# Performance work log

Measured on AMD Instinct MI355X. Metric: run time of the kernel, lower is better.

The kernel has to match this reference:

```python
import jax, jax.numpy as jnp
import numpy as np

B, R, D, H = 8192, 6, 1024, 256
TEMP = 0.5
SINKHORN_ITERS = 5


def rmsnorm(x, g, eps=1e-6):
    return x * jax.lax.rsqrt(jnp.mean(x * x, axis=-1, keepdims=True) + eps) * g


def setup_inputs() -> dict:
    key = jax.random.key(0)
    ks = jax.random.split(key, 24)
    def p(k, shape, fan):
        return jax.random.normal(k, shape, jnp.float32) / np.float32(np.sqrt(fan))
    return {
        'source_roles': jax.random.normal(ks[0], (B, R, D), jnp.float32),
        'target_roles': jax.random.normal(ks[1], (B, R, D), jnp.float32),
        # role_encoder: Linear(D,H) -> RMSNorm(H) -> SwiGLU(H, 2H) -> Linear(H,H)
        'W1': p(ks[2], (H, D), D), 'b1': jnp.zeros((H,), jnp.float32),
        'g1': jnp.ones((H,), jnp.float32),
        'Wa': p(ks[3], (2 * H, H), H),  # SwiGLU gate proj
        'Wb': p(ks[4], (2 * H, H), H),  # SwiGLU value proj
        'Wc': p(ks[5], (H, 2 * H), 2 * H),  # SwiGLU down proj
        'W2': p(ks[6], (H, H), H), 'b2': jnp.zeros((H,), jnp.float32),
        # map_score: Bilinear(H, H, 1)
        'Wbil': p(ks[7], (H, H), H), 'bbil': jnp.zeros((1,), jnp.float32),
        # answer_proj: Linear(2H,2H) -> GELU -> Linear(2H,D) -> RMSNorm(D)
        'Wa1': p(ks[8], (2 * H, 2 * H), 2 * H), 'ba1': jnp.zeros((2 * H,), jnp.float32),
        'Wa2': p(ks[9], (D, 2 * H), 2 * H), 'ba2': jnp.zeros((D,), jnp.float32),
        'g2': jnp.ones((D,), jnp.float32),
        # confidence_head: Linear(1,1) -> Sigmoid (input is a scalar statistic per batch)
        'Wc1': p(ks[10], (1, 1), 1), 'bc1': jnp.zeros((1,), jnp.float32),
    }


def reference(source_roles, target_roles, W1, b1, g1, Wa, Wb, Wc, W2, b2,
              Wbil, bbil, Wa1, ba1, Wa2, ba2, g2, Wc1, bc1):
    def role_encoder(x):  # [B,R,D] -> [B,R,H]
        x = x @ W1.T + b1
        x = rmsnorm(x, g1)
        x = (jax.nn.silu(x @ Wa.T) * (x @ Wb.T)) @ Wc.T  # SwiGLU
        return x @ W2.T + b2

    src_enc = role_encoder(source_roles)  # [B,R,H]
    tgt_enc = role_encoder(target_roles)  # [B,R,H]

    # Bilinear pairwise score: [B, R_src, R_tgt]
    log_alpha = (jnp.einsum('bih,hk,bjk->bij', src_enc, Wbil, tgt_enc) + bbil) / TEMP

    def sinkhorn_step(la, _):
        la = la - jax.nn.logsumexp(la, axis=-1, keepdims=True)
        la = la - jax.nn.logsumexp(la, axis=-2, keepdims=True)
        return la, None

    log_alpha, _ = jax.lax.scan(sinkhorn_step, log_alpha, None, length=SINKHORN_ITERS)
    mapping = jnp.exp(log_alpha)  # doubly-stochastic [B,R,R]

    mapped_src = jnp.einsum('bij,bjh->bih', mapping, tgt_enc)  # [B,R,H]

    diff = jnp.mean(jnp.abs(mapped_src - src_enc), axis=-1, keepdims=True)  # [B,R,1]
    conf_in = jnp.mean(diff, axis=-2)  # [B,1]
    confidence = jax.nn.sigmoid(conf_in @ Wc1.T + bc1).squeeze(-1)  # [B]

    combined = jnp.concatenate([mapped_src, tgt_enc], axis=-1)  # [B,R,2H]
    a = jax.nn.gelu(combined @ Wa1.T + ba1)
    answer = rmsnorm(a @ Wa2.T + ba2, g2)  # [B,R,D]
    return answer, mapping, mapped_src, confidence
```

## Files before the change

kernel.cpp:

```cpp
#include <hip/hip_runtime.h>
#include <hip/hip_bf16.h>


typedef float f32x4 __attribute__((ext_vector_type(4)));
typedef short s16x8 __attribute__((ext_vector_type(8)));
typedef short s16x4 __attribute__((ext_vector_type(4)));

__device__ __forceinline__ unsigned short f2bf(float x) {
  unsigned int u = __float_as_uint(x);
  u += 0x7FFFu + ((u >> 16) & 1u);
  return (unsigned short)(u >> 16);
}
__device__ __forceinline__ float bf2f(unsigned short b) {
  return __uint_as_float(((unsigned int)b) << 16);
}

enum { A_F32 = 0, A_PLANES = 1, A_BF16 = 2, A_CAT = 3 };
enum { E_NONE = 0, E_GELU = 1, E_SILUMUL = 2 };
enum { O_F32 = 0, O_PLANES = 1, O_BF16 = 2 };

template<int AIN, bool SPLIT, int EPI, int OUT>
__global__ __launch_bounds__(256, 2)
void gemm2(const float* __restrict__ Af,
           const short* __restrict__ Ahi, const short* __restrict__ Alo,
           const short* __restrict__ Acat2,
           const short* __restrict__ Whi, const short* __restrict__ Wlo,
           const float* __restrict__ bias,
           float* __restrict__ Cf, short* __restrict__ Chi, short* __restrict__ Clo,
           const short* __restrict__ Xhi, const short* __restrict__ Xlo,
           int K, int N)
{
  constexpr int BM = 128, BN = 128, BK = 64;
  __shared__ __attribute__((aligned(16))) short sAhi[BM * BK];
  __shared__ __attribute__((aligned(16))) short sBhi[BN * BK];
  __shared__ __attribute__((aligned(16))) short sAlo[SPLIT ? BM * BK : 8];
  __shared__ __attribute__((aligned(16))) short sBlo[SPLIT ? BN * BK : 8];

  const int tid = threadIdx.x;
  const int n0 = blockIdx.x * BN;
  const int m0 = blockIdx.y * BM;
  const int lane = tid & 63, w = tid >> 6;
  const int wr = (w >> 1) * 64, wc = (w & 1) * 64;

  f32x4 acc[4][4] = {};

  for (int k0 = 0; k0 < K; k0 += BK) {
    __syncthreads();
    if (AIN == A_F32) {
#pragma unroll
      for (int it = 0; it < 8; ++it) {
        int f = it * 256 + tid;
        int r = f >> 4, q = f & 15;
        f32x4 v = *reinterpret_cast<const f32x4*>(Af + (size_t)(m0 + r) * K + k0 + q * 4);
        s16x4 hi, lo;
#pragma unroll
        for (int j = 0; j < 4; ++j) {
          unsigned short h = f2bf(v[j]);
          hi[j] = (short)h;
          if (SPLIT) lo[j] = (short)f2bf(v[j] - bf2f(h));
        }
        int off = r * 64 + (((q >> 1) ^ (r & 7)) << 3) + ((q & 1) << 2);
        *reinterpret_cast<s16x4*>(&sAhi[off]) = hi;
        if (SPLIT) *reinterpret_cast<s16x4*>(&sAlo[off]) = lo;
      }
    } else {
#pragma unroll
      for (int it = 0; it < 4; ++it) {
        int c = it * 256 + tid;
        int r = c >> 3, ch = c & 7;
        int off = r * 64 + ((ch ^ (r & 7)) << 3);
        const short* srcHi = nullptr; const short* srcLo = nullptr;
        if (AIN == A_PLANES || AIN == A_BF16) {
          size_t g = (size_t)(m0 + r) * K + k0 + ch * 8;
          srcHi = Ahi + g;
          if (SPLIT) srcLo = Alo + g;
        } else {
          int kk = k0 + ch * 8;
          srcHi = (kk < 256) ? (Ahi + (size_t)(m0 + r) * 256 + kk)
                             : (Acat2 + (size_t)(m0 + r) * 256 + (kk - 256));
        }
        *reinterpret_cast<s16x8*>(&sAhi[off]) = *reinterpret_cast<const s16x8*>(srcHi);
        if (SPLIT) *reinterpret_cast<s16x8*>(&sAlo[off]) = *reinterpret_cast<const s16x8*>(srcLo);
      }
    }
#pragma unroll
    for (int it = 0; it < 4; ++it) {
      int c = it * 256 + tid;
      int r = c >> 3, ch = c & 7;
      size_t g = (size_t)(n0 + r) * K + k0 + ch * 8;
      int off = r * 64 + ((ch ^ (r & 7)) << 3);
      *reinterpret_cast<s16x8*>(&sBhi[off]) = *reinterpret_cast<const s16x8*>(Whi + g);
      if (SPLIT) *reinterpret_cast<s16x8*>(&sBlo[off]) = *reinterpret_cast<const s16x8*>(Wlo + g);
    }
    __syncthreads();
#pragma unroll
    for (int kc = 0; kc < 2; ++kc) {
      s16x8 ah[4], al[4];
#pragma unroll
      for (int mt = 0; mt < 4; ++mt) {
        int r = wr + mt * 16 + (lane & 15);
        int off = r * 64 + ((((kc << 2) + (lane >> 4)) ^ (r & 7)) << 3);
        ah[mt] = *reinterpret_cast<const s16x8*>(&sAhi[off]);
        if (SPLIT) al[mt] = *reinterpret_cast<const s16x8*>(&sAlo[off]);
      }
#pragma unroll
      for (int nt = 0; nt < 4; ++nt) {
        int r = wc + nt * 16 + (lane & 15);
        int off = r * 64 + ((((kc << 2) + (lane >> 4)) ^ (r & 7)) << 3);
        s16x8 bh = *reinterpret_cast<const s16x8*>(&sBhi[off]);
        s16x8 bl = {};
        if (SPLIT) bl = *reinterpret_cast<const s16x8*>(&sBlo[off]);
#pragma unroll
        for (int mt = 0; mt < 4; ++mt) {
          acc[mt][nt] = __builtin_amdgcn_mfma_f32_16x16x32_bf16(ah[mt], bh, acc[mt][nt], 0, 0, 0);
          if (SPLIT) {
            acc[mt][nt] = __builtin_amdgcn_mfma_f32_16x16x32_bf16(ah[mt], bl, acc[mt][nt], 0, 0, 0);
            acc[mt][nt] = __builtin_amdgcn_mfma_f32_16x16x32_bf16(al[mt], bh, acc[mt][nt], 0, 0, 0);
          }
        }
      }
    }
  }
#pragma unroll
  for (int mt = 0; mt < 4; ++mt) {
#pragma unroll
    for (int nt = 0; nt < 4; ++nt) {
      int cc = n0 + wc + nt * 16 + (lane & 15);
      float bv = bias ? bias[cc] : 0.f;
#pragma unroll
      for (int j = 0; j < 4; ++j) {
        int rr = m0 + wr + mt * 16 + (lane >> 4) * 4 + j;
        float v = acc[mt][nt][j] + bv;
        size_t idx = (size_t)rr * N + cc;
        if (EPI == E_GELU) {
          float x3 = v * v * v;
          v = 0.5f * v * (1.f + tanhf(0.7978845608028654f * (v + 0.044715f * x3)));
        } else if (EPI == E_SILUMUL) {
          float xa = bf2f((unsigned short)Xhi[idx]) + bf2f((unsigned short)Xlo[idx]);
          v *= xa / (1.f + expf(-xa));
        }
        if (OUT == O_F32) {
          Cf[idx] = v;
        } else if (OUT == O_BF16) {
          Chi[idx] = (short)f2bf(v);
        } else {
          unsigned short hh = f2bf(v);
          Chi[idx] = (short)hh;
          Clo[idx] = (short)f2bf(v - bf2f(hh));
        }
      }
    }
  }
}

__global__ __launch_bounds__(256)
void prep_w(const float* __restrict__ W1, const float* __restrict__ Wa,
            const float* __restrict__ Wb, const float* __restrict__ Wc,
            const float* __restrict__ W2, const float* __restrict__ Wbil,
            const float* __restrict__ Wa1, const float* __restrict__ Wa2,
            short* __restrict__ hi, short* __restrict__ lo)
{
  int e0 = (blockIdx.x * 256 + threadIdx.x) * 4;
  const float* src; int local; bool tr = false;
  if      (e0 < 262144)  { src = W1;   local = e0; }
  else if (e0 < 393216)  { src = Wa;   local = e0 - 262144; }
  else if (e0 < 524288)  { src = Wb;   local = e0 - 393216; }
  else if (e0 < 655360)  { src = Wc;   local = e0 - 524288; }
  else if (e0 < 720896)  { src = W2;   local = e0 - 655360; }
  else if (e0 < 786432)  { src = Wbil; local = e0 - 720896; tr = true; }
  else if (e0 < 1048576) { src = Wa1;  local = e0 - 786432; }
  else                   { src = Wa2;  local = e0 - 1048576; }
  float v[4];
  if (tr) {
#pragma unroll
    for (int t = 0; t < 4; ++t) {
      int li = local + t;
      int n = li >> 8, hh = li & 255;
      v[t] = src[hh * 256 + n];
    }
  } else {
    f32x4 tv = *reinterpret_cast<const f32x4*>(src + local);
    v[0] = tv[0]; v[1] = tv[1]; v[2] = tv[2]; v[3] = tv[3];
  }
#pragma unroll
  for (int t = 0; t < 4; ++t) {
    unsigned short h = f2bf(v[t]);
    hi[e0 + t] = (short)h;
    lo[e0 + t] = (short)f2bf(v[t] - bf2f(h));
  }
}

__global__ __launch_bounds__(256)
void rmsnorm_planes256(short* __restrict__ xhi, short* __restrict__ xlo,
                       const float* __restrict__ g)
{
  int wid = threadIdx.x >> 6, lane = threadIdx.x & 63;
  size_t row = (size_t)blockIdx.x * 4 + wid;
  short* ph = xhi + row * 256 + lane * 4;
  short* pl = xlo + row * 256 + lane * 4;
  s16x4 h4 = *reinterpret_cast<const s16x4*>(ph);
  s16x4 l4 = *reinterpret_cast<const s16x4*>(pl);
  float v[4]; float ss = 0.f;
#pragma unroll
  for (int j = 0; j < 4; ++j) {
    v[j] = bf2f((unsigned short)h4[j]) + bf2f((unsigned short)l4[j]);
    ss += v[j] * v[j];
  }
#pragma unroll
  for (int o = 32; o > 0; o >>= 1) ss += __shfl_xor(ss, o);
  float s = rsqrtf(ss * (1.f / 256.f) + 1e-6f);
  f32x4 gg = *reinterpret_cast<const f32x4*>(g + lane * 4);
#pragma unroll
  for (int j = 0; j < 4; ++j) {
    float o = v[j] * s * gg[j];
    unsigned short hh = f2bf(o);
    h4[j] = (short)hh;
    l4[j] = (short)f2bf(o - bf2f(hh));
  }
  *reinterpret_cast<s16x4*>(ph) = h4;
  *reinterpret_cast<s16x4*>(pl) = l4;
}

__global__ __launch_bounds__(256)
void rmsnorm_f32_1024(float* __restrict__ x, const float* __restrict__ g)
{
  constexpr int NV = 4;
  int wid = threadIdx.x >> 6, lane = threadIdx.x & 63;
  size_t row = (size_t)blockIdx.x * 4 + wid;
  float* p = x + row * 1024;
  f32x4 v[NV];
  float ss = 0.f;
#pragma unroll
  for (int i = 0; i < NV; ++i) {
    v[i] = *reinterpret_cast<const f32x4*>(p + (i * 64 + lane) * 4);
    ss += v[i][0] * v[i][0] + v[i][1] * v[i][1] + v[i][2] * v[i][2] + v[i][3] * v[i][3];
  }
#pragma unroll
  for (int o = 32; o > 0; o >>= 1) ss += __shfl_xor(ss, o);
  float s = rsqrtf(ss * (1.f / 1024.f) + 1e-6f);
#pragma unroll
  for (int i = 0; i < NV; ++i) {
    f32x4 gg = *reinterpret_cast<const f32x4*>(g + (i * 64 + lane) * 4);
    f32x4 o4;
#pragma unroll
    for (int j = 0; j < 4; ++j) o4[j] = v[i][j] * s * gg[j];
    *reinterpret_cast<f32x4*>(p + (i * 64 + lane) * 4) = o4;
  }
}

__global__ __launch_bounds__(64)
void sinkhorn_k(const float* __restrict__ P,
                const short* __restrict__ Sehi, const short* __restrict__ Selo,
                const short* __restrict__ Tehi, const short* __restrict__ Telo,
                const float* __restrict__ bbil,
                const float* __restrict__ Wc1, const float* __restrict__ bc1,
                float* __restrict__ omap, float* __restrict__ omapped,
                short* __restrict__ omappedb, float* __restrict__ oconf)
{
  int b = blockIdx.x, lane = threadIdx.x;
  __shared__ __attribute__((aligned(16))) float sP[6 * 260];
  __shared__ __attribute__((aligned(16))) float sT[6 * 260];
  __shared__ __attribute__((aligned(16))) float sS[6 * 260];
  const f32x4* gp = reinterpret_cast<const f32x4*>(P + (size_t)b * 1536);
#pragma unroll
  for (int i0 = 0; i0 < 6; ++i0) {
    int i = i0 * 64 + lane;
    int r = i >> 6, c = i & 63;
    *reinterpret_cast<f32x4*>(&sP[r * 260 + c * 4]) = gp[i];
    size_t e = (size_t)b * 1536 + i * 4;
    s16x4 th = *reinterpret_cast<const s16x4*>(Tehi + e);
    s16x4 tl = *reinterpret_cast<const s16x4*>(Telo + e);
    s16x4 sh = *reinterpret_cast<const s16x4*>(Sehi + e);
    s16x4 sl = *reinterpret_cast<const s16x4*>(Selo + e);
#pragma unroll
    for (int j = 0; j < 4; ++j) {
      sT[r * 260 + c * 4 + j] = bf2f((unsigned short)th[j]) + bf2f((unsigned short)tl[j]);
      sS[r * 260 + c * 4 + j] = bf2f((unsigned short)sh[j]) + bf2f((unsigned short)sl[j]);
    }
  }
  __syncthreads();
  int i = lane / 6, j = lane - i * 6;
  float la = 0.f;
  if (lane < 36) {
    const float* pr = &sP[i * 260];
    const float* tr = &sT[j * 260];
    float d = 0.f;
    for (int k = 0; k < 256; ++k) d = fmaf(pr[k], tr[k], d);
    la = (d + bbil[0]) * 2.0f;
  }
#pragma unroll
  for (int it = 0; it < 5; ++it) {
    float m = -1e30f, s = 0.f;
#pragma unroll
    for (int t = 0; t < 6; ++t) m = fmaxf(m, __shfl(la, i * 6 + t));
#pragma unroll
    for (int t = 0; t < 6; ++t) s += expf(__shfl(la, i * 6 + t) - m);
    la -= m + logf(s);
    m = -1e30f; s = 0.f;
#pragma unroll
    for (int t = 0; t < 6; ++t) m = fmaxf(m, __shfl(la, t * 6 + j));
#pragma unroll
    for (int t = 0; t < 6; ++t) s += expf(__shfl(la, t * 6 + j) - m);
    la -= m + logf(s);
  }
  float mp = (lane < 36) ? expf(la) : 0.f;
  if (lane < 36) omap[(size_t)b * 36 + lane] = mp;
  float mm[36];
#pragma unroll
  for (int t = 0; t < 36; ++t) mm[t] = __shfl(mp, t);
  float asum = 0.f;
#pragma unroll
  for (int ii = 0; ii < 6; ++ii) {
    f32x4 av = {0.f, 0.f, 0.f, 0.f};
#pragma unroll
    for (int k = 0; k < 6; ++k) {
      f32x4 tv = *reinterpret_cast<const f32x4*>(&sT[k * 260 + lane * 4]);
      av += tv * mm[ii * 6 + k];
    }
    f32x4 sv = *reinterpret_cast<const f32x4*>(&sS[ii * 260 + lane * 4]);
    size_t e = (size_t)b * 1536 + ii * 256 + lane * 4;
    *reinterpret_cast<f32x4*>(omapped + e) = av;
    s16x4 mb;
#pragma unroll
    for (int jj = 0; jj < 4; ++jj) mb[jj] = (short)f2bf(av[jj]);
    *reinterpret_cast<s16x4*>(omappedb + e) = mb;
    asum += fabsf(av[0] - sv[0]) + fabsf(av[1] - sv[1]) +
            fabsf(av[2] - sv[2]) + fabsf(av[3] - sv[3]);
  }
#pragma unroll
  for (int o = 32; o > 0; o >>= 1) asum += __shfl_xor(asum, o);
  if (lane == 0) {
    float ci = asum * (1.f / 1536.f);
    float z = ci * Wc1[0] + bc1[0];
    oconf[b] = 1.f / (1.f + expf(-z));
  }
}

extern "C" void kernel_launch(void* const* d_in, const int* in_sizes, int n_in,
                              void* d_out, int out_size, void* d_ws, size_t ws_size,
                              hipStream_t stream)
{
  const float* src_roles = (const float*)d_in[0];
  const float* tgt_roles = (const float*)d_in[1];
  const float* W1   = (const float*)d_in[2];
  const float* b1   = (const float*)d_in[3];
  const float* g1   = (const float*)d_in[4];
  const float* Wa   = (const float*)d_in[5];
  const float* Wb   = (const float*)d_in[6];
  const float* Wc   = (const float*)d_in[7];
  const float* W2   = (const float*)d_in[8];
  const float* b2   = (const float*)d_in[9];
  const float* Wbil = (const float*)d_in[10];
  const float* bbil = (const float*)d_in[11];
  const float* Wa1  = (const float*)d_in[12];
  const float* ba1  = (const float*)d_in[13];
  const float* Wa2  = (const float*)d_in[14];
  const float* ba2  = (const float*)d_in[15];
  const float* g2   = (const float*)d_in[16];
  const float* Wc1  = (const float*)d_in[17];
  const float* bc1  = (const float*)d_in[18];

  float* out = (float*)d_out;
  float* o_answer  = out;
  float* o_mapping = out + 50331648;
  float* o_mapped  = out + 50626560;
  float* o_conf    = out + 63209472;
  short* xa_hi = (short*)out;
  short* xa_lo = xa_hi + 25165824;
  short* t_hi  = xa_lo + 25165824;
  short* t_lo  = t_hi + 25165824;

  float* P = (float*)d_ws;
  short* sb = (short*)((float*)d_ws + 12582912);
  short* whi  = sb;
  short* wlo  = whi + 1572864;
  short* h_hi = wlo + 1572864;
  short* h_lo = h_hi + 12582912;
  short* u_hi = h_lo + 12582912;
  short* u_lo = u_hi + 12582912;
  short* eS_hi = u_lo + 12582912;
  short* eS_lo = eS_hi + 12582912;
  short* eT_hi = eS_lo + 12582912;
  short* eT_lo = eT_hi + 12582912;
  short* act   = eT_lo + 12582912;
  short* mapb  = act + 25165824;

  const int oW1 = 0, oWa = 262144, oWb = 393216, oWc = 524288, oW2 = 655360,
            oWbt = 720896, oWa1 = 786432, oWa2 = 1048576;
  const short* NS = nullptr; const float* NF = nullptr;
  float* NFo = nullptr; short* NSo = nullptr;

  hipLaunchKernelGGL(prep_w, dim3(1536), dim3(256), 0, stream,
                     W1, Wa, Wb, Wc, W2, Wbil, Wa1, Wa2, whi, wlo);

  for (int s = 0; s < 2; ++s) {
    const float* X = (s == 0) ? src_roles : tgt_roles;
    short* e_hi = (s == 0) ? eS_hi : eT_hi;
    short* e_lo = (s == 0) ? eS_lo : eT_lo;
    hipLaunchKernelGGL((gemm2<A_F32, true, E_NONE, O_PLANES>), dim3(2, 384), dim3(256), 0, stream,
                       X, NS, NS, NS, whi + oW1, wlo + oW1, b1, NFo, h_hi, h_lo, NS, NS, 1024, 256);
    hipLaunchKernelGGL(rmsnorm_planes256, dim3(12288), dim3(256), 0, stream, h_hi, h_lo, g1);
    hipLaunchKernelGGL((gemm2<A_PLANES, true, E_NONE, O_PLANES>), dim3(4, 384), dim3(256), 0, stream,
                       NF, h_hi, h_lo, NS, whi + oWa, wlo + oWa, NF, NFo, xa_hi, xa_lo, NS, NS, 256, 512);
    hipLaunchKernelGGL((gemm2<A_PLANES, true, E_SILUMUL, O_PLANES>), dim3(4, 384), dim3(256), 0, stream,
                       NF, h_hi, h_lo, NS, whi + oWb, wlo + oWb, NF, NFo, t_hi, t_lo, xa_hi, xa_lo, 256, 512);
    hipLaunchKernelGGL((gemm2<A_PLANES, true, E_NONE, O_PLANES>), dim3(2, 384), dim3(256), 0, stream,
                       NF, t_hi, t_lo, NS, whi + oWc, wlo + oWc, NF, NFo, u_hi, u_lo, NS, NS, 512, 256);
    hipLaunchKernelGGL((gemm2<A_PLANES, true, E_NONE, O_PLANES>), dim3(2, 384), dim3(256), 0, stream,
                       NF, u_hi, u_lo, NS, whi + oW2, wlo + oW2, b2, NFo, e_hi, e_lo, NS, NS, 256, 256);
  }
  hipLaunchKernelGGL((gemm2<A_PLANES, true, E_NONE, O_F32>), dim3(2, 384), dim3(256), 0, stream,
                     NF, eS_hi, eS_lo, NS, whi + oWbt, wlo + oWbt, NF, P, NSo, NSo, NS, NS, 256, 256);
  hipLaunchKernelGGL(sinkhorn_k, dim3(8192), dim3(64), 0, stream,
                     P, eS_hi, eS_lo, eT_hi, eT_lo, bbil, Wc1, bc1,
                     o_mapping, o_mapped, mapb, o_conf);
  hipLaunchKernelGGL((gemm2<A_CAT, false, E_GELU, O_BF16>), dim3(4, 384), dim3(256), 0, stream,
                     NF, mapb, NS, eT_hi, whi + oWa1, wlo + oWa1, ba1, NFo, act, NSo, NS, NS, 512, 512);
  hipLaunchKernelGGL((gemm2<A_BF16, false, E_NONE, O_F32>), dim3(8, 384), dim3(256), 0, stream,
                     NF, act, NS, NS, whi + oWa2, wlo + oWa2, ba2, o_answer, NSo, NSo, NS, NS, 512, 1024);
  hipLaunchKernelGGL(rmsnorm_f32_1024, dim3(12288), dim3(256), 0, stream, o_answer, g2);
}
```

Baseline: 1.436 ms.

## Use direct global-to-LDS loads, pre-split inputs, batch first GEMM, swizzle block order

The GEMM now stages tiles with global_load_lds (16-byte direct-to-LDS loads) in place of register round-trips. The XOR bank swizzle is dropped because those loads write fixed contiguous slabs. The f32-to-bf16 hi/lo split of the inputs moves into a separate split_x pass, so the first GEMM and its RMSNorm run once over both source and target batches. Workgroup IDs are remapped in strides of 8, apparently to group blocks across XCDs for cache locality. The cost is an extra full write and read of the split inputs, plus possible LDS bank conflicts now that the swizzle is gone.

```diff
diff --git a/kernel.cpp b/kernel.cpp
--- a/kernel.cpp
+++ b/kernel.cpp
@@ -15,14 +15,18 @@
   return __uint_as_float(((unsigned int)b) << 16);
 }
 
-enum { A_F32 = 0, A_PLANES = 1, A_BF16 = 2, A_CAT = 3 };
+__device__ __forceinline__ void gl16(const void* g, void* l) {
+  __builtin_amdgcn_global_load_lds((const __attribute__((address_space(1))) void*)g,
+                                   (__attribute__((address_space(3))) void*)l,
+                                   16, 0, 0);
+}
+
 enum { E_NONE = 0, E_GELU = 1, E_SILUMUL = 2 };
 enum { O_F32 = 0, O_PLANES = 1, O_BF16 = 2 };
 
-template<int AIN, bool SPLIT, int EPI, int OUT>
+template<bool SPLIT, int EPI, int OUT, bool CAT>
 __global__ __launch_bounds__(256, 2)
-void gemm2(const float* __restrict__ Af,
-           const short* __restrict__ Ahi, const short* __restrict__ Alo,
+void gemm3(const short* __restrict__ Ahi, const short* __restrict__ Alo,
            const short* __restrict__ Acat2,
            const short* __restrict__ Whi, const short* __restrict__ Wlo,
            const float* __restrict__ bias,
@@ -36,77 +40,52 @@
   __shared__ __attribute__((aligned(16))) short sAlo[SPLIT ? BM * BK : 8];
   __shared__ __attribute__((aligned(16))) short sBlo[SPLIT ? BN * BK : 8];
 
+  const int nwg = gridDim.x * gridDim.y;
+  const int bid = blockIdx.y * gridDim.x + blockIdx.x;
+  const int logical = (bid & 7) * (nwg >> 3) + (bid >> 3);
+  const int bx = logical % gridDim.x, by = logical / gridDim.x;
+  const int n0 = bx * BN, m0 = by * BM;
+
   const int tid = threadIdx.x;
-  const int n0 = blockIdx.x * BN;
-  const int m0 = blockIdx.y * BM;
   const int lane = tid & 63, w = tid >> 6;
   const int wr = (w >> 1) * 64, wc = (w & 1) * 64;
+  const int slr = lane >> 3, slc = lane & 7;
 
   f32x4 acc[4][4] = {};
 
   for (int k0 = 0; k0 < K; k0 += BK) {
     __syncthreads();
-    if (AIN == A_F32) {
-#pragma unroll
-      for (int it = 0; it < 8; ++it) {
-        int f = it * 256 + tid;
-        int r = f >> 4, q = f & 15;
-        f32x4 v = *reinterpret_cast<const f32x4*>(Af + (size_t)(m0 + r) * K + k0 + q * 4);
-        s16x4 hi, lo;
-#pragma unroll
-        for (int j = 0; j < 4; ++j) {
-          unsigned short h = f2bf(v[j]);
-          hi[j] = (short)h;
-          if (SPLIT) lo[j] = (short)f2bf(v[j] - bf2f(h));
-        }
-        int off = r * 64 + (((q >> 1) ^ (r & 7)) << 3) + ((q & 1) << 2);
-        *reinterpret_cast<s16x4*>(&sAhi[off]) = hi;
-        if (SPLIT) *reinterpret_cast<s16x4*>(&sAlo[off]) = lo;
+#pragma unroll
+    for (int s4 = 0; s4 < 4; ++s4) {
+      const int slab = (w << 2) + s4;
+      const int ar = slab * 8 + slr;
+      const short* ga;
+      if (CAT) {
+        const short* base = (k0 < 256) ? Ahi : Acat2;
+        const int kk = (k0 < 256) ? k0 : (k0 - 256);
+        ga = base + (size_t)(m0 + ar) * 256 + kk + slc * 8;
+      } else {
+        ga = Ahi + (size_t)(m0 + ar) * K + k0 + slc * 8;
       }
-    } else {
-#pragma unroll
-      for (int it = 0; it < 4; ++it) {
-        int c = it * 256 + tid;
-        int r = c >> 3, ch = c & 7;
-        int off = r * 64 + ((ch ^ (r & 7)) << 3);
-        const short* srcHi = nullptr; const short* srcLo = nullptr;
-        if (AIN == A_PLANES || AIN == A_BF16) {
-          size_t g = (size_t)(m0 + r) * K + k0 + ch * 8;
-          srcHi = Ahi + g;
-          if (SPLIT) srcLo = Alo + g;
-        } else {
-          int kk = k0 + ch * 8;
-          srcHi = (kk < 256) ? (Ahi + (size_t)(m0 + r) * 256 + kk)
-                             : (Acat2 + (size_t)(m0 + r) * 256 + (kk - 256));
-        }
-        *reinterpret_cast<s16x8*>(&sAhi[off]) = *reinterpret_cast<const s16x8*>(srcHi);
-        if (SPLIT) *reinterpret_cast<s16x8*>(&sAlo[off]) = *reinterpret_cast<const s16x8*>(srcLo);
-      }
-    }
-#pragma unroll
-    for (int it = 0; it < 4; ++it) {
-      int c = it * 256 + tid;
-      int r = c >> 3, ch = c & 7;
-      size_t g = (size_t)(n0 + r) * K + k0 + ch * 8;
-      int off = r * 64 + ((ch ^ (r & 7)) << 3);
-      *reinterpret_cast<s16x8*>(&sBhi[off]) = *reinterpret_cast<const s16x8*>(Whi + g);
-      if (SPLIT) *reinterpret_cast<s16x8*>(&sBlo[off]) = *reinterpret_cast<const s16x8*>(Wlo + g);
+      gl16(ga, &sAhi[slab * 512]);
+      if (SPLIT) gl16(Alo + (size_t)(m0 + ar) * K + k0 + slc * 8, &sAlo[slab * 512]);
+      gl16(Whi + (size_t)(n0 + ar) * K + k0 + slc * 8, &sBhi[slab * 512]);
+      if (SPLIT) gl16(Wlo + (size_t)(n0 + ar) * K + k0 + slc * 8, &sBlo[slab * 512]);
     }
     __syncthreads();
 #pragma unroll
     for (int kc = 0; kc < 2; ++kc) {
+      const int c8 = ((kc << 2) + (lane >> 4)) * 8;
       s16x8 ah[4], al[4];
 #pragma unroll
       for (int mt = 0; mt < 4; ++mt) {
-        int r = wr + mt * 16 + (lane & 15);
-        int off = r * 64 + ((((kc << 2) + (lane >> 4)) ^ (r & 7)) << 3);
+        const int off = (wr + mt * 16 + (lane & 15)) * 64 + c8;
         ah[mt] = *reinterpret_cast<const s16x8*>(&sAhi[off]);
         if (SPLIT) al[mt] = *reinterpret_cast<const s16x8*>(&sAlo[off]);
       }
 #pragma unroll
       for (int nt = 0; nt < 4; ++nt) {
-        int r = wc + nt * 16 + (lane & 15);
-        int off = r * 64 + ((((kc << 2) + (lane >> 4)) ^ (r & 7)) << 3);
+        const int off = (wc + nt * 16 + (lane & 15)) * 64 + c8;
         s16x8 bh = *reinterpret_cast<const s16x8*>(&sBhi[off]);
         s16x8 bl = {};
         if (SPLIT) bl = *reinterpret_cast<const s16x8*>(&sBlo[off]);
@@ -125,13 +104,13 @@
   for (int mt = 0; mt < 4; ++mt) {
 #pragma unroll
     for (int nt = 0; nt < 4; ++nt) {
-      int cc = n0 + wc + nt * 16 + (lane & 15);
-      float bv = bias ? bias[cc] : 0.f;
+      const int cc = n0 + wc + nt * 16 + (lane & 15);
+      const float bv = bias ? bias[cc] : 0.f;
 #pragma unroll
       for (int j = 0; j < 4; ++j) {
-        int rr = m0 + wr + mt * 16 + (lane >> 4) * 4 + j;
+        const int rr = m0 + wr + mt * 16 + (lane >> 4) * 4 + j;
         float v = acc[mt][nt][j] + bv;
-        size_t idx = (size_t)rr * N + cc;
+        const size_t idx = (size_t)rr * N + cc;
         if (EPI == E_GELU) {
           float x3 = v * v * v;
           v = 0.5f * v * (1.f + tanhf(0.7978845608028654f * (v + 0.044715f * x3)));
@@ -154,6 +133,27 @@
 }
 
 __global__ __launch_bounds__(256)
+void split_x(const float* __restrict__ xs, const float* __restrict__ xt,
+             short* __restrict__ hi, short* __restrict__ lo)
+{
+  const size_t half4 = 12582912;
+  for (size_t i4 = (size_t)blockIdx.x * 256 + threadIdx.x; i4 < 25165824;
+       i4 += (size_t)gridDim.x * 256) {
+    const float* src = (i4 < half4) ? (xs + i4 * 4) : (xt + (i4 - half4) * 4);
+    f32x4 v = *reinterpret_cast<const f32x4*>(src);
+    s16x4 h4, l4;
+#pragma unroll
+    for (int j = 0; j < 4; ++j) {
+      unsigned short h = f2bf(v[j]);
+      h4[j] = (short)h;
+      l4[j] = (short)f2bf(v[j] - bf2f(h));
+    }
+    *reinterpret_cast<s16x4*>(hi + i4 * 4) = h4;
+    *reinterpret_cast<s16x4*>(lo + i4 * 4) = l4;
+  }
+}
+
+__global__ __launch_bounds__(256)
 void prep_w(const float* __restrict__ W1, const float* __restrict__ Wa,
             const float* __restrict__ Wb, const float* __restrict__ Wc,
             const float* __restrict__ W2, const float* __restrict__ Wbil,
@@ -224,14 +224,13 @@
 __global__ __launch_bounds__(256)
 void rmsnorm_f32_1024(float* __restrict__ x, const float* __restrict__ g)
 {
-  constexpr int NV = 4;
   int wid = threadIdx.x >> 6, lane = threadIdx.x & 63;
   size_t row = (size_t)blockIdx.x * 4 + wid;
   float* p = x + row * 1024;
-  f32x4 v[NV];
+  f32x4 v[4];
   float ss = 0.f;
 #pragma unroll
-  for (int i = 0; i < NV; ++i) {
+  for (int i = 0; i < 4; ++i) {
     v[i] = *reinterpret_cast<const f32x4*>(p + (i * 64 + lane) * 4);
     ss += v[i][0] * v[i][0] + v[i][1] * v[i][1] + v[i][2] * v[i][2] + v[i][3] * v[i][3];
   }
@@ -239,7 +238,7 @@
   for (int o = 32; o > 0; o >>= 1) ss += __shfl_xor(ss, o);
   float s = rsqrtf(ss * (1.f / 1024.f) + 1e-6f);
 #pragma unroll
-  for (int i = 0; i < NV; ++i) {
+  for (int i = 0; i < 4; ++i) {
     f32x4 gg = *reinterpret_cast<const f32x4*>(g + (i * 64 + lane) * 4);
     f32x4 o4;
 #pragma unroll
@@ -370,20 +369,22 @@
   short* t_hi  = xa_lo + 25165824;
   short* t_lo  = t_hi + 25165824;
 
-  float* P = (float*)d_ws;
-  short* sb = (short*)((float*)d_ws + 12582912);
-  short* whi  = sb;
-  short* wlo  = whi + 1572864;
-  short* h_hi = wlo + 1572864;
-  short* h_lo = h_hi + 12582912;
-  short* u_hi = h_lo + 12582912;
-  short* u_lo = u_hi + 12582912;
-  short* eS_hi = u_lo + 12582912;
-  short* eS_lo = eS_hi + 12582912;
-  short* eT_hi = eS_lo + 12582912;
-  short* eT_lo = eT_hi + 12582912;
-  short* act   = eT_lo + 12582912;
-  short* mapb  = act + 25165824;
+  short* S = (short*)d_ws;
+  short* Xp_hi = S;
+  short* Xp_lo = S + 100663296;
+  short* u_hi  = S + 0;
+  short* u_lo  = S + 12582912;
+  short* eS_hi = S + 25165824;
+  short* eS_lo = S + 37748736;
+  short* eT_hi = S + 50331648;
+  short* eT_lo = S + 62914560;
+  short* act   = S + 75497472;
+  short* mapb  = S + 100663296;
+  float* P     = (float*)(S + 201326592);
+  short* whi   = S + 226492416;
+  short* wlo   = S + 228065280;
+  short* h_hi  = S + 229638144;
+  short* h_lo  = S + 254803968;
 
   const int oW1 = 0, oWa = 262144, oWb = 393216, oWc = 524288, oW2 = 655360,
             oWbt = 720896, oWa1 = 786432, oWa2 = 1048576;
@@ -392,31 +393,43 @@
 
   hipLaunchKernelGGL(prep_w, dim3(1536), dim3(256), 0, stream,
                      W1, Wa, Wb, Wc, W2, Wbil, Wa1, Wa2, whi, wlo);
+  hipLaunchKernelGGL(split_x, dim3(2048), dim3(256), 0, stream,
+                     src_roles, tgt_roles, Xp_hi, Xp_lo);
+
+  hipLaunchKernelGGL((gemm3<true, E_NONE, O_PLANES, false>), dim3(2, 768), dim3(256), 0, stream,
+                     Xp_hi, Xp_lo, NS, whi + oW1, wlo + oW1, b1,
+                     NFo, h_hi, h_lo, NS, NS, 1024, 256);
+  hipLaunchKernelGGL(rmsnorm_planes256, dim3(24576), dim3(256), 0, stream, h_hi, h_lo, g1);
 
   for (int s = 0; s < 2; ++s) {
-    const float* X = (s == 0) ? src_roles : tgt_roles;
+    const short* hs_hi = h_hi + (size_t)s * 49152 * 256;
+    const short* hs_lo = h_lo + (size_t)s * 49152 * 256;
     short* e_hi = (s == 0) ? eS_hi : eT_hi;
     short* e_lo = (s == 0) ? eS_lo : eT_lo;
-    hipLaunchKernelGGL((gemm2<A_F32, true, E_NONE, O_PLANES>), dim3(2, 384), dim3(256), 0, stream,
-                       X, NS, NS, NS, whi + oW1, wlo + oW1, b1, NFo, h_hi, h_lo, NS, NS, 1024, 256);
-    hipLaunchKernelGGL(rmsnorm_planes256, dim3(12288), dim3(256), 0, stream, h_hi, h_lo, g1);
-    hipLaunchKernelGGL((gemm2<A_PLANES, true, E_NONE, O_PLANES>), dim3(4, 384), dim3(256), 0, stream,
-                       NF, h_hi, h_lo, NS, whi + oWa, wlo + oWa, NF, NFo, xa_hi, xa_lo, NS, NS, 256, 512);
-    hipLaunchKernelGGL((gemm2<A_PLANES, true, E_SILUMUL, O_PLANES>), dim3(4, 384), dim3(256), 0, stream,
-                       NF, h_hi, h_lo, NS, whi + oWb, wlo + oWb, NF, NFo, t_hi, t_lo, xa_hi, xa_lo, 256, 512);
-    hipLaunchKernelGGL((gemm2<A_PLANES, true, E_NONE, O_PLANES>), dim3(2, 384), dim3(256), 0, stream,
-                       NF, t_hi, t_lo, NS, whi + oWc, wlo + oWc, NF, NFo, u_hi, u_lo, NS, NS, 512, 256);
-    hipLaunchKernelGGL((gemm2<A_PLANES, true, E_NONE, O_PLANES>), dim3(2, 384), dim3(256), 0, stream,
-                       NF, u_hi, u_lo, NS, whi + oW2, wlo + oW2, b2, NFo, e_hi, e_lo, NS, NS, 256, 256);
-  }
-  hipLaunchKernelGGL((gemm2<A_PLANES, true, E_NONE, O_F32>), dim3(2, 384), dim3(256), 0, stream,
-                     NF, eS_hi, eS_lo, NS, whi + oWbt, wlo + oWbt, NF, P, NSo, NSo, NS, NS, 256, 256);
+    hipLaunchKernelGGL((gemm3<true, E_NONE, O_PLANES, false>), dim3(4, 384), dim3(256), 0, stream,
+                       hs_hi, hs_lo, NS, whi + oWa, wlo + oWa, NF,
+                       NFo, xa_hi, xa_lo, NS, NS, 256, 512);
+    hipLaunchKernelGGL((gemm3<true, E_SILUMUL, O_PLANES, false>), dim3(4, 384), dim3(256), 0, stream,
+                       hs_hi, hs_lo, NS, whi + oWb, wlo + oWb, NF,
+                       NFo, t_hi, t_lo, xa_hi, xa_lo, 256, 512);
+    hipLaunchKernelGGL((gemm3<true, E_NONE, O_PLANES, false>), dim3(2, 384), dim3(256), 0, stream,
+                       t_hi, t_lo, NS, whi + oWc, wlo + oWc, NF,
+                       NFo, u_hi, u_lo, NS, NS, 512, 256);
+    hipLaunchKernelGGL((gemm3<true, E_NONE, O_PLANES, false>), dim3(2, 384), dim3(256), 0, stream,
+                       u_hi, u_lo, NS, whi + oW2, wlo + oW2, b2,
+                       NFo, e_hi, e_lo, NS, NS, 256, 256);
+  }
+  hipLaunchKernelGGL((gemm3<true, E_NONE, O_F32, false>), dim3(2, 384), dim3(256), 0, stream,
+                     eS_hi, eS_lo, NS, whi + oWbt, wlo + oWbt, NF,
+                     P, NSo, NSo, NS, NS, 256, 256);
   hipLaunchKernelGGL(sinkhorn_k, dim3(8192), dim3(64), 0, stream,
                      P, eS_hi, eS_lo, eT_hi, eT_lo, bbil, Wc1, bc1,
                      o_mapping, o_mapped, mapb, o_conf);
-  hipLaunchKernelGGL((gemm2<A_CAT, false, E_GELU, O_BF16>), dim3(4, 384), dim3(256), 0, stream,
-                     NF, mapb, NS, eT_hi, whi + oWa1, wlo + oWa1, ba1, NFo, act, NSo, NS, NS, 512, 512);
-  hipLaunchKernelGGL((gemm2<A_BF16, false, E_NONE, O_F32>), dim3(8, 384), dim3(256), 0, stream,
-                     NF, act, NS, NS, whi + oWa2, wlo + oWa2, ba2, o_answer, NSo, NSo, NS, NS, 512, 1024);
+  hipLaunchKernelGGL((gemm3<false, E_GELU, O_BF16, true>), dim3(4, 384), dim3(256), 0, stream,
+                     mapb, NS, eT_hi, whi + oWa1, wlo + oWa1, ba1,
+                     NFo, act, NSo, NS, NS, 512, 512);
+  hipLaunchKernelGGL((gemm3<false, E_NONE, O_F32, false>), dim3(8, 384), dim3(256), 0, stream,
+                     act, NS, NS, whi + oWa2, wlo + oWa2, ba2,
+                     o_answer, NSo, NSo, NS, NS, 512, 1024);
   hipLaunchKernelGGL(rmsnorm_f32_1024, dim3(12288), dim3(256), 0, stream, o_answer, g2);
 }
```

Result: slower. 1.572 ms (+9.5%).
